# Optimization experiments

Measured on AMD Instinct MI355X. Metric: run time of the kernel, lower is better.

## Reference

```python
import jax, jax.numpy as jnp
import numpy as np

N = 10000
IN_DIM = 1024
HID = 128
LAT = 64
E = 320000


def setup_inputs() -> dict:
    key = jax.random.key(0)
    ks = jax.random.split(key, 12)
    def glorot(k, shape):
        lim = float(np.sqrt(6.0 / (shape[0] + shape[1])))
        return jax.random.uniform(k, shape, jnp.float32, -lim, lim)
    x = jax.random.normal(ks[0], (N, IN_DIM), jnp.float32)
    edge_index = jax.random.randint(ks[1], (2, E), 0, N, jnp.int64)
    return {
        "x": x,
        "edge_index": edge_index,
        "W_enc1": glorot(ks[2], (IN_DIM, HID)), "b_enc1": jnp.zeros((HID,), jnp.float32),
        "W_enc2": glorot(ks[3], (HID, LAT)),   "b_enc2": jnp.zeros((LAT,), jnp.float32),
        "W_att1": glorot(ks[4], (LAT, HID)),   "b_att1": jnp.zeros((HID,), jnp.float32),
        "W_att2": glorot(ks[5], (HID, IN_DIM)),"b_att2": jnp.zeros((IN_DIM,), jnp.float32),
        "W_str":  glorot(ks[6], (LAT, LAT)),   "b_str":  jnp.zeros((LAT,), jnp.float32),
    }


def _gcn_norm(edge_index, n):
    # PyG GCNConv default: add self-loops, symmetric normalization
    loop = jnp.arange(n, dtype=edge_index.dtype)
    send = jnp.concatenate([edge_index[0], loop])
    recv = jnp.concatenate([edge_index[1], loop])
    deg = jax.ops.segment_sum(jnp.ones_like(recv, dtype=jnp.float32), recv, num_segments=n)
    dis = jnp.where(deg > 0, jax.lax.rsqrt(deg), 0.0)
    norm = dis[send] * dis[recv]  # [E+N]
    return send, recv, norm


def _gcn(x, W, b, send, recv, norm, n):
    h = x @ W                                  # [N, out]
    msg = h[send] * norm[:, None]              # gather + scale
    agg = jax.ops.segment_sum(msg, recv, num_segments=n)  # scatter-add
    return agg + b


def reference(x, edge_index, W_enc1, b_enc1, W_enc2, b_enc2,
              W_att1, b_att1, W_att2, b_att2, W_str, b_str):
    n = x.shape[0]
    send, recv, norm = _gcn_norm(edge_index, n)
    # encoder
    h = jax.nn.relu(_gcn(x, W_enc1, b_enc1, send, recv, norm, n))
    z = jax.nn.relu(_gcn(h, W_enc2, b_enc2, send, recv, norm, n))
    # attribute decoder
    a = jax.nn.relu(_gcn(z, W_att1, b_att1, send, recv, norm, n))
    attr_recon = jax.nn.relu(_gcn(a, W_att2, b_att2, send, recv, norm, n))
    # structure decoder
    s = jax.nn.relu(_gcn(z, W_str, b_str, send, recv, norm, n))
    struct_recon = s @ s.T  # [N, N]
    return (attr_recon, struct_recon, z)
```

## Files before the change

### kernel.cpp

```cpp
#include <hip/hip_runtime.h>
#include <hip/hip_bf16.h>

#define IN_DIM 1024
#define HID 128
#define LAT 64
#define DEGPAD 128

typedef __attribute__((ext_vector_type(8))) short bf16x8;
typedef __attribute__((ext_vector_type(4))) short bf16x4;
typedef __attribute__((ext_vector_type(4))) float f32x4;

#define W1T_OFF 0
#define W2T_OFF 131072
#define Wa1T_OFF 139264
#define Wa2T_OFF 147456
#define WsT_OFF 278528
#define WT_TOTAL 282624

__device__ __forceinline__ void splitf(float v, __hip_bfloat16& h, __hip_bfloat16& l) {
    h = __float2bfloat16(v);
    l = __float2bfloat16(v - __bfloat162float(h));
}


template<int AMODE, bool BIAS, bool RELU, bool DIS, bool SPLITOUT, bool NT>
__device__ void dev_gemm(float* smem, int bx, int byy,
        const __hip_bfloat16* __restrict__ Ahi, const __hip_bfloat16* __restrict__ Alo,
        const float* __restrict__ Af,
        const __hip_bfloat16* __restrict__ Bthi, const __hip_bfloat16* __restrict__ Btlo,
        const float* __restrict__ bias, const int* __restrict__ cursor,
        float* __restrict__ Cf, __hip_bfloat16* __restrict__ Chi, __hip_bfloat16* __restrict__ Clo,
        int M, int K, int ldc) {
    int tid = threadIdx.x;
    int w = tid >> 6, lane = tid & 63;
    int wr = w >> 1, wc = w & 1;
    int m0 = byy * 128, n0 = bx * 64;
    int lrow = lane & 15, lk = (lane >> 4) * 8;

    int arow[4];
    size_t aoff[4];
#pragma unroll
    for (int mi = 0; mi < 4; ++mi) {
        arow[mi] = m0 + wr * 64 + mi * 16 + lrow;
        aoff[mi] = (size_t)arow[mi] * K + lk;
    }
    size_t boff[2];
#pragma unroll
    for (int nj = 0; nj < 2; ++nj)
        boff[nj] = (size_t)(n0 + wc * 32 + nj * 16 + lrow) * K + lk;

    f32x4 acc[4][2] = {};

    for (int k0 = 0; k0 < K; k0 += 32) {
        bf16x8 bh[2], bl[2], ah[4], al[4];
#pragma unroll
        for (int nj = 0; nj < 2; ++nj) {
            bh[nj] = *(const bf16x8*)(Bthi + boff[nj] + k0);
            bl[nj] = *(const bf16x8*)(Btlo + boff[nj] + k0);
        }
        if constexpr (AMODE == 0) {
#pragma unroll
            for (int mi = 0; mi < 4; ++mi) {
                ah[mi] = *(const bf16x8*)(Ahi + aoff[mi] + k0);
                al[mi] = *(const bf16x8*)(Alo + aoff[mi] + k0);
            }
        } else {
#pragma unroll
            for (int mi = 0; mi < 4; ++mi) {
                float4 f0 = make_float4(0.f, 0.f, 0.f, 0.f), f1 = f0;
                if (arow[mi] < M) {
                    f0 = *(const float4*)(Af + aoff[mi] + k0);
                    f1 = *(const float4*)(Af + aoff[mi] + k0 + 4);
                }
                float ff[8] = {f0.x, f0.y, f0.z, f0.w, f1.x, f1.y, f1.z, f1.w};
                __attribute__((aligned(16))) __hip_bfloat16 hb[8], lb[8];
#pragma unroll
                for (int t = 0; t < 8; ++t) splitf(ff[t], hb[t], lb[t]);
                ah[mi] = *(const bf16x8*)hb;
                al[mi] = *(const bf16x8*)lb;
            }
        }
#pragma unroll
        for (int mi = 0; mi < 4; ++mi)
#pragma unroll
            for (int nj = 0; nj < 2; ++nj) {
                acc[mi][nj] = __builtin_amdgcn_mfma_f32_16x16x32_bf16(ah[mi], bh[nj], acc[mi][nj], 0, 0, 0);
                acc[mi][nj] = __builtin_amdgcn_mfma_f32_16x16x32_bf16(ah[mi], bl[nj], acc[mi][nj], 0, 0, 0);
                acc[mi][nj] = __builtin_amdgcn_mfma_f32_16x16x32_bf16(al[mi], bh[nj], acc[mi][nj], 0, 0, 0);
            }
    }

    int r0 = (lane >> 4) * 4;
#pragma unroll
    for (int mi = 0; mi < 4; ++mi)
#pragma unroll
        for (int nj = 0; nj < 2; ++nj) {
            int cl = wc * 32 + nj * 16 + lrow;
#pragma unroll
            for (int r = 0; r < 4; ++r) {
                int rl = wr * 64 + mi * 16 + r0 + r;
                smem[rl * 68 + cl] = acc[mi][nj][r];
            }
        }
    __syncthreads();

#pragma unroll
    for (int it = 0; it < 8; ++it) {
        int rl = it * 16 + (tid >> 4);
        int c4 = tid & 15;
        int row = m0 + rl;
        if (row < M) {
            int col = n0 + c4 * 4;
            float4 v = *(const float4*)&smem[rl * 68 + c4 * 4];
            if (BIAS) {
                float4 b = *(const float4*)&bias[col];
                v.x += b.x; v.y += b.y; v.z += b.z; v.w += b.w;
            }
            if (RELU) {
                v.x = fmaxf(v.x, 0.f); v.y = fmaxf(v.y, 0.f);
                v.z = fmaxf(v.z, 0.f); v.w = fmaxf(v.w, 0.f);
            }
            if (DIS) {
                float di = rsqrtf((float)(cursor[row] + 1));
                v.x *= di; v.y *= di; v.z *= di; v.w *= di;
            }
            if constexpr (SPLITOUT) {
                float vv[4] = {v.x, v.y, v.z, v.w};
                __attribute__((aligned(8))) __hip_bfloat16 hs[4], ls[4];
#pragma unroll
                for (int k = 0; k < 4; ++k) splitf(vv[k], hs[k], ls[k]);
                *(bf16x4*)&Chi[(size_t)row * ldc + col] = *(bf16x4*)hs;
                *(bf16x4*)&Clo[(size_t)row * ldc + col] = *(bf16x4*)ls;
            } else if constexpr (NT) {
                __builtin_nontemporal_store(*(const f32x4*)&v, (f32x4*)&Cf[(size_t)row * ldc + col]);
            } else {
                *(float4*)&Cf[(size_t)row * ldc + col] = v;
            }
        }
    }
    __syncthreads();
}


__device__ void dev_sst(float* smem, int bi, int bj,
                        const __hip_bfloat16* __restrict__ Shi, const __hip_bfloat16* __restrict__ Slo,
                        float* __restrict__ C, int M) {
    int tid = threadIdx.x;
    int w = tid >> 6, lane = tid & 63;
    int wr = w >> 1, wc = w & 1;
    int i0 = bi * 128 + wr * 64;
    int j0 = bj * 128 + wc * 64;
    int lrow = lane & 15, lk = (lane >> 4) * 8;

    f32x4 acc[4][4] = {};
#pragma unroll
    for (int ks = 0; ks < 2; ++ks) {
        bf16x8 ah[4], al[4], bh[4], bl[4];
#pragma unroll
        for (int mi = 0; mi < 4; ++mi) {
            size_t off = (size_t)(i0 + mi * 16 + lrow) * 64 + ks * 32 + lk;
            ah[mi] = *(const bf16x8*)(Shi + off);
            al[mi] = *(const bf16x8*)(Slo + off);
        }
#pragma unroll
        for (int nj = 0; nj < 4; ++nj) {
            size_t off = (size_t)(j0 + nj * 16 + lrow) * 64 + ks * 32 + lk;
            bh[nj] = *(const bf16x8*)(Shi + off);
            bl[nj] = *(const bf16x8*)(Slo + off);
        }
#pragma unroll
        for (int mi = 0; mi < 4; ++mi)
#pragma unroll
            for (int nj = 0; nj < 4; ++nj) {
                acc[mi][nj] = __builtin_amdgcn_mfma_f32_16x16x32_bf16(ah[mi], bh[nj], acc[mi][nj], 0, 0, 0);
                acc[mi][nj] = __builtin_amdgcn_mfma_f32_16x16x32_bf16(ah[mi], bl[nj], acc[mi][nj], 0, 0, 0);
                acc[mi][nj] = __builtin_amdgcn_mfma_f32_16x16x32_bf16(al[mi], bh[nj], acc[mi][nj], 0, 0, 0);
            }
    }

    int r0 = (lane >> 4) * 4;

    if (bi != bj) {
#pragma unroll
        for (int mi = 0; mi < 4; ++mi)
#pragma unroll
            for (int nj = 0; nj < 4; ++nj) {
                int orow = j0 + nj * 16 + lrow;
                int ocol = i0 + mi * 16 + r0;
                if (orow < M && ocol < M) {
                    f32x4 v = acc[mi][nj];
                    __builtin_nontemporal_store(v, (f32x4*)&C[(size_t)orow * M + ocol]);
                }
            }
    }

#pragma unroll
    for (int p = 0; p < 2; ++p) {
        if (wc == p) {
#pragma unroll
            for (int mi = 0; mi < 4; ++mi)
#pragma unroll
                for (int nj = 0; nj < 4; ++nj) {
                    int cl = nj * 16 + lrow;
#pragma unroll
                    for (int r = 0; r < 4; ++r) {
                        int rl = wr * 64 + mi * 16 + r0 + r;
                        smem[rl * 68 + cl] = acc[mi][nj][r];
                    }
                }
        }
        __syncthreads();
#pragma unroll
        for (int it = 0; it < 8; ++it) {
            int rl = it * 16 + (tid >> 4);
            int c4 = tid & 15;
            int row = bi * 128 + rl;
            int col = bj * 128 + p * 64 + c4 * 4;
            if (row < M && col < M) {
                float4 v = *(const float4*)&smem[rl * 68 + c4 * 4];
                __builtin_nontemporal_store(*(const f32x4*)&v, (f32x4*)&C[(size_t)row * M + col]);
            }
        }
        __syncthreads();
    }
}


__global__ __launch_bounds__(256) void k_prep(const float* __restrict__ W1, const float* __restrict__ W2,
                                              const float* __restrict__ Wa1, const float* __restrict__ Wa2,
                                              const float* __restrict__ Ws,
                                              __hip_bfloat16* __restrict__ hi, __hip_bfloat16* __restrict__ lo,
                                              int* cursor, int N) {
    int gtid = blockIdx.x * 256 + threadIdx.x;
    int gsz = gridDim.x * 256;
    for (int i = gtid; i < N; i += gsz) cursor[i] = 0;
    for (int idx = gtid; idx < WT_TOTAL; idx += gsz) {
        const float* src; int base, shK, Nc;
        if (idx < W2T_OFF)       { src = W1;  base = W1T_OFF;  shK = 10; Nc = 128; }
        else if (idx < Wa1T_OFF) { src = W2;  base = W2T_OFF;  shK = 7;  Nc = 64; }
        else if (idx < Wa2T_OFF) { src = Wa1; base = Wa1T_OFF; shK = 6;  Nc = 128; }
        else if (idx < WsT_OFF)  { src = Wa2; base = Wa2T_OFF; shK = 7;  Nc = 1024; }
        else                     { src = Ws;  base = WsT_OFF;  shK = 6;  Nc = 64; }
        int local = idx - base;
        int nn = local >> shK;
        int k = local & ((1 << shK) - 1);
        splitf(src[(size_t)k * Nc + nn], hi[idx], lo[idx]);
    }
}

__global__ __launch_bounds__(256) void k_build(const int* __restrict__ ei, int* cursor,
                                               int* __restrict__ colPad, int E,
                                               const float* __restrict__ x,
                                               const __hip_bfloat16* __restrict__ Whi,
                                               const __hip_bfloat16* __restrict__ Wlo,
                                               float* __restrict__ t128, int M, int Mpad) {
    __shared__ float smem[128 * 68];
    int gtid = blockIdx.x * 256 + threadIdx.x;
    int gsz = gridDim.x * 256;
    for (int e = gtid; e < E; e += gsz) {
        int s = ei[e], r = ei[E + e];
        int slot = atomicAdd(&cursor[r], 1);
        if (slot < DEGPAD) colPad[(size_t)r * DEGPAD + slot] = s;
    }
    int nt2 = (Mpad / 128) * 2;
    for (int t = blockIdx.x; t < nt2; t += gridDim.x)
        dev_gemm<1, false, false, false, false, false>(smem, t & 1, t >> 1,
            nullptr, nullptr, x, Whi + W1T_OFF, Wlo + W1T_OFF, nullptr, nullptr,
            t128, nullptr, nullptr, M, 1024, 128);
}

template<int F, bool BIAS, bool RELU, int OMODE, bool GD>
__global__ __launch_bounds__(256) void k_spmm(const float* __restrict__ Hin,
                                              const int* __restrict__ colPad,
                                              const int* __restrict__ cursor,
                                              const float* __restrict__ bias,
                                              float* __restrict__ out, float* __restrict__ out2,
                                              __hip_bfloat16* __restrict__ ohi,
                                              __hip_bfloat16* __restrict__ olo, int n) {
    constexpr int JW = F / 64;
    int i = (blockIdx.x * 256 + threadIdx.x) >> 6;
    int lane = threadIdx.x & 63;
    if (i >= n) return;
    int d = cursor[i];
    float di = rsqrtf((float)(d + 1));
    if (d > DEGPAD) d = DEGPAD;
    const int* cp = colPad + (size_t)i * DEGPAD;
    float acc[JW];
    const float* self = Hin + (size_t)i * F;
#pragma unroll
    for (int j = 0; j < JW; ++j) acc[j] = (GD ? di : 1.f) * self[lane + 64 * j];

    int p = 0;
    for (; p + 4 <= d; p += 4) {
        int4 cidx = *(const int4*)(cp + p);
        int cc[4] = {cidx.x, cidx.y, cidx.z, cidx.w};
        float dc[4];
        if constexpr (GD) {
#pragma unroll
            for (int q = 0; q < 4; ++q) dc[q] = rsqrtf((float)(cursor[cc[q]] + 1));
        }
        float vals[4][JW];
#pragma unroll
        for (int q = 0; q < 4; ++q) {
            const float* row = Hin + (size_t)cc[q] * F;
#pragma unroll
            for (int j = 0; j < JW; ++j) vals[q][j] = row[lane + 64 * j];
        }
#pragma unroll
        for (int q = 0; q < 4; ++q)
#pragma unroll
            for (int j = 0; j < JW; ++j)
                acc[j] = GD ? fmaf(dc[q], vals[q][j], acc[j]) : (acc[j] + vals[q][j]);
    }
    for (; p < d; ++p) {
        int c = cp[p];
        const float* row = Hin + (size_t)c * F;
        if constexpr (GD) {
            float dc = rsqrtf((float)(cursor[c] + 1));
#pragma unroll
            for (int j = 0; j < JW; ++j) acc[j] = fmaf(dc, row[lane + 64 * j], acc[j]);
        } else {
#pragma unroll
            for (int j = 0; j < JW; ++j) acc[j] += row[lane + 64 * j];
        }
    }

#pragma unroll
    for (int j = 0; j < JW; ++j) {
        float r = acc[j] * di;
        if (BIAS) r += bias[lane + 64 * j];
        if (RELU) r = fmaxf(r, 0.f);
        size_t idx = (size_t)i * F + lane + 64 * j;
        if constexpr (OMODE == 1) {
            __hip_bfloat16 h, l;
            splitf(r, h, l);
            ohi[idx] = h; olo[idx] = l;
        } else {
            out[idx] = r;
            if constexpr (OMODE == 2) out2[idx] = r * di;
        }
    }
}

__global__ __launch_bounds__(256) void k_g2(const __hip_bfloat16* __restrict__ Hhi,
                                            const __hip_bfloat16* __restrict__ Hlo,
                                            const __hip_bfloat16* __restrict__ Whi,
                                            const __hip_bfloat16* __restrict__ Wlo,
                                            const int* __restrict__ cursor,
                                            float* __restrict__ t64, int M) {
    __shared__ float smem[128 * 68];
    dev_gemm<0, false, false, true, false, false>(smem, 0, blockIdx.x,
        Hhi, Hlo, nullptr, Whi + W2T_OFF, Wlo + W2T_OFF, nullptr, cursor,
        t64, nullptr, nullptr, M, 128, 64);
}

__global__ __launch_bounds__(256) void k_g34(const __hip_bfloat16* __restrict__ AZhi,
                                             const __hip_bfloat16* __restrict__ AZlo,
                                             const __hip_bfloat16* __restrict__ Whi,
                                             const __hip_bfloat16* __restrict__ Wlo,
                                             const float* __restrict__ ba1, const float* __restrict__ bs,
                                             const int* __restrict__ cursor,
                                             float* __restrict__ t128,
                                             __hip_bfloat16* __restrict__ Shi, __hip_bfloat16* __restrict__ Slo,
                                             int M, int Mpad) {
    __shared__ float smem[128 * 68];
    int nt2 = (Mpad / 128) * 2;
    int t = blockIdx.x;
    if (t < nt2)
        dev_gemm<0, true, true, true, false, false>(smem, t & 1, t >> 1,
            AZhi, AZlo, nullptr, Whi + Wa1T_OFF, Wlo + Wa1T_OFF, ba1, cursor,
            t128, nullptr, nullptr, M, 64, 128);
    else
        dev_gemm<0, true, true, false, true, false>(smem, 0, t - nt2,
            AZhi, AZlo, nullptr, Whi + WsT_OFF, Wlo + WsT_OFF, bs, nullptr,
            nullptr, Shi, Slo, M, 64, 64);
}

__global__ __launch_bounds__(256) void k_tail(const __hip_bfloat16* __restrict__ AAhi,
                                              const __hip_bfloat16* __restrict__ AAlo,
                                              const __hip_bfloat16* __restrict__ Whi,
                                              const __hip_bfloat16* __restrict__ Wlo,
                                              const float* __restrict__ ba2,
                                              const __hip_bfloat16* __restrict__ Shi,
                                              const __hip_bfloat16* __restrict__ Slo,
                                              float* __restrict__ attr, float* __restrict__ st,
                                              int M, int Mpad) {
    __shared__ float smem[128 * 68];
    int nt = Mpad / 128;
    int nG5 = 16 * nt;
    int t = blockIdx.x;
    if (t < nG5) {
        dev_gemm<0, true, true, false, false, true>(smem, t & 15, t >> 4,
            AAhi, AAlo, nullptr, Whi + Wa2T_OFF, Wlo + Wa2T_OFF, ba2, nullptr,
            attr, nullptr, nullptr, M, 128, 1024);
    } else {
        int tt = t - nG5;
        int bi = 0;
        while (tt >= nt - bi) { tt -= nt - bi; bi++; }
        dev_sst(smem, bi, bi + tt, Shi, Slo, st, M);
    }
}


extern "C" void kernel_launch(void* const* d_in, const int* in_sizes, int n_in,
                              void* d_out, int out_size, void* d_ws, size_t ws_size,
                              hipStream_t stream) {
    const float* x   = (const float*)d_in[0];
    const int*   ei  = (const int*)d_in[1];
    const float* W1  = (const float*)d_in[2];
    const float* b1  = (const float*)d_in[3];
    const float* W2  = (const float*)d_in[4];
    const float* b2  = (const float*)d_in[5];
    const float* Wa1 = (const float*)d_in[6];
    const float* ba1 = (const float*)d_in[7];
    const float* Wa2 = (const float*)d_in[8];
    const float* ba2 = (const float*)d_in[9];
    const float* Ws  = (const float*)d_in[10];
    const float* bs  = (const float*)d_in[11];

    int N = in_sizes[0] / IN_DIM;
    int E = in_sizes[1] / 2;
    int Mpad = ((N + 127) / 128) * 128;
    int nt = Mpad / 128;

    float* out  = (float*)d_out;
    float* attr = out;
    float* st   = out + (size_t)N * IN_DIM;
    float* zout = st + (size_t)N * N;

    char* basep = (char*)d_ws;
    size_t off = 0;
    auto alloc = [&](size_t bytes) -> void* {
        void* p = basep + off;
        off = (off + bytes + 255) & ~(size_t)255;
        return p;
    };
    int*   colPad = (int*)alloc((size_t)N * DEGPAD * 4);
    int*   cursor = (int*)alloc((size_t)N * 4);
    __hip_bfloat16* Whi = (__hip_bfloat16*)alloc((size_t)WT_TOTAL * 2);
    __hip_bfloat16* Wlo = (__hip_bfloat16*)alloc((size_t)WT_TOTAL * 2);
    float* t128 = (float*)alloc((size_t)N * 128 * 4);
    float* t64  = (float*)alloc((size_t)N * 64 * 4);
    float* zp   = (float*)alloc((size_t)N * 64 * 4);
    __hip_bfloat16* Hhi  = (__hip_bfloat16*)alloc((size_t)Mpad * 128 * 2);
    __hip_bfloat16* Hlo  = (__hip_bfloat16*)alloc((size_t)Mpad * 128 * 2);
    __hip_bfloat16* AZhi = (__hip_bfloat16*)alloc((size_t)Mpad * 64 * 2);
    __hip_bfloat16* AZlo = (__hip_bfloat16*)alloc((size_t)Mpad * 64 * 2);
    __hip_bfloat16* AAhi = (__hip_bfloat16*)alloc((size_t)Mpad * 128 * 2);
    __hip_bfloat16* AAlo = (__hip_bfloat16*)alloc((size_t)Mpad * 128 * 2);
    __hip_bfloat16* Shi  = (__hip_bfloat16*)alloc((size_t)Mpad * 64 * 2);
    __hip_bfloat16* Slo  = (__hip_bfloat16*)alloc((size_t)Mpad * 64 * 2);

    dim3 b256(256);
    int spmm_grid = (N * 64 + 255) / 256;

    k_prep<<<dim3(1104), b256, 0, stream>>>(W1, W2, Wa1, Wa2, Ws, Whi, Wlo, cursor, N);
    k_build<<<dim3(1280), b256, 0, stream>>>(ei, cursor, colPad, E, x, Whi, Wlo, t128, N, Mpad);
    k_spmm<128, true, true, 1, true><<<dim3(spmm_grid), b256, 0, stream>>>(
        t128, colPad, cursor, b1, nullptr, nullptr, Hhi, Hlo, N);
    k_g2<<<dim3(nt), b256, 0, stream>>>(Hhi, Hlo, Whi, Wlo, cursor, t64, N);
    k_spmm<64, true, true, 2, false><<<dim3(spmm_grid), b256, 0, stream>>>(
        t64, colPad, cursor, b2, zout, zp, nullptr, nullptr, N);
    k_spmm<64, false, false, 1, false><<<dim3(spmm_grid), b256, 0, stream>>>(
        zp, colPad, cursor, nullptr, nullptr, nullptr, AZhi, AZlo, N);
    k_g34<<<dim3(3 * nt), b256, 0, stream>>>(AZhi, AZlo, Whi, Wlo, ba1, bs, cursor, t128, Shi, Slo, N, Mpad);
    k_spmm<128, false, false, 1, false><<<dim3(spmm_grid), b256, 0, stream>>>(
        t128, colPad, cursor, nullptr, nullptr, nullptr, AAhi, AAlo, N);
    k_tail<<<dim3(16 * nt + nt * (nt + 1) / 2), b256, 0, stream>>>(
        AAhi, AAlo, Whi, Wlo, ba2, Shi, Slo, attr, st, N, Mpad);
}
```

Before: 300.0 us.

## Move edge CSR build into prep and fold degree scaling into first GEMM epilogue

The edge bucketing with atomics moves from the build kernel into the weight-prep kernel, and the cursor zeroing becomes a memset. The first layer's GEMM becomes its own kernel that applies the source-degree scale through its epilogue (the flag that takes cursor). This removes the per-neighbour rsqrt and cursor gather from the first SpMM. The SpMM also gets an 8-wide unrolled gather loop for more memory-level parallelism. It costs an extra launch and a stricter ordering between the CSR build and the GEMM.

Result: no change. 299.7 us (median of 2 runs) (-0.1%).

```diff
diff --git a/kernel.cpp b/kernel.cpp
--- a/kernel.cpp
+++ b/kernel.cpp
@@ -230,10 +230,15 @@
                                               const float* __restrict__ Wa1, const float* __restrict__ Wa2,
                                               const float* __restrict__ Ws,
                                               __hip_bfloat16* __restrict__ hi, __hip_bfloat16* __restrict__ lo,
-                                              int* cursor, int N) {
+                                              const int* __restrict__ ei, int* cursor,
+                                              int* __restrict__ colPad, int E) {
     int gtid = blockIdx.x * 256 + threadIdx.x;
     int gsz = gridDim.x * 256;
-    for (int i = gtid; i < N; i += gsz) cursor[i] = 0;
+    for (int e = gtid; e < E; e += gsz) {
+        int s = ei[e], r = ei[E + e];
+        int slot = atomicAdd(&cursor[r], 1);
+        if (slot < DEGPAD) colPad[(size_t)r * DEGPAD + slot] = s;
+    }
     for (int idx = gtid; idx < WT_TOTAL; idx += gsz) {
         const float* src; int base, shK, Nc;
         if (idx < W2T_OFF)       { src = W1;  base = W1T_OFF;  shK = 10; Nc = 128; }
@@ -248,28 +253,19 @@
     }
 }
 
-__global__ __launch_bounds__(256) void k_build(const int* __restrict__ ei, int* cursor,
-                                               int* __restrict__ colPad, int E,
-                                               const float* __restrict__ x,
-                                               const __hip_bfloat16* __restrict__ Whi,
-                                               const __hip_bfloat16* __restrict__ Wlo,
-                                               float* __restrict__ t128, int M, int Mpad) {
+__global__ __launch_bounds__(256) void k_g1(const float* __restrict__ x,
+                                            const __hip_bfloat16* __restrict__ Whi,
+                                            const __hip_bfloat16* __restrict__ Wlo,
+                                            const int* __restrict__ cursor,
+                                            float* __restrict__ t128, int M) {
     __shared__ float smem[128 * 68];
-    int gtid = blockIdx.x * 256 + threadIdx.x;
-    int gsz = gridDim.x * 256;
-    for (int e = gtid; e < E; e += gsz) {
-        int s = ei[e], r = ei[E + e];
-        int slot = atomicAdd(&cursor[r], 1);
-        if (slot < DEGPAD) colPad[(size_t)r * DEGPAD + slot] = s;
-    }
-    int nt2 = (Mpad / 128) * 2;
-    for (int t = blockIdx.x; t < nt2; t += gridDim.x)
-        dev_gemm<1, false, false, false, false, false>(smem, t & 1, t >> 1,
-            nullptr, nullptr, x, Whi + W1T_OFF, Wlo + W1T_OFF, nullptr, nullptr,
-            t128, nullptr, nullptr, M, 1024, 128);
-}
-
-template<int F, bool BIAS, bool RELU, int OMODE, bool GD>
+    int t = blockIdx.x;
+    dev_gemm<1, false, false, true, false, false>(smem, t & 1, t >> 1,
+        nullptr, nullptr, x, Whi + W1T_OFF, Wlo + W1T_OFF, nullptr, cursor,
+        t128, nullptr, nullptr, M, 1024, 128);
+}
+
+template<int F, bool BIAS, bool RELU, int OMODE>
 __global__ __launch_bounds__(256) void k_spmm(const float* __restrict__ Hin,
                                               const int* __restrict__ colPad,
                                               const int* __restrict__ cursor,
@@ -288,17 +284,28 @@
     float acc[JW];
     const float* self = Hin + (size_t)i * F;
 #pragma unroll
-    for (int j = 0; j < JW; ++j) acc[j] = (GD ? di : 1.f) * self[lane + 64 * j];
+    for (int j = 0; j < JW; ++j) acc[j] = self[lane + 64 * j];
 
     int p = 0;
+    for (; p + 8 <= d; p += 8) {
+        int4 ca = *(const int4*)(cp + p);
+        int4 cb = *(const int4*)(cp + p + 4);
+        int cc[8] = {ca.x, ca.y, ca.z, ca.w, cb.x, cb.y, cb.z, cb.w};
+        float vals[8][JW];
+#pragma unroll
+        for (int q = 0; q < 8; ++q) {
+            const float* row = Hin + (size_t)cc[q] * F;
+#pragma unroll
+            for (int j = 0; j < JW; ++j) vals[q][j] = row[lane + 64 * j];
+        }
+#pragma unroll
+        for (int q = 0; q < 8; ++q)
+#pragma unroll
+            for (int j = 0; j < JW; ++j) acc[j] += vals[q][j];
+    }
     for (; p + 4 <= d; p += 4) {
-        int4 cidx = *(const int4*)(cp + p);
-        int cc[4] = {cidx.x, cidx.y, cidx.z, cidx.w};
-        float dc[4];
-        if constexpr (GD) {
-#pragma unroll
-            for (int q = 0; q < 4; ++q) dc[q] = rsqrtf((float)(cursor[cc[q]] + 1));
-        }
+        int4 ca = *(const int4*)(cp + p);
+        int cc[4] = {ca.x, ca.y, ca.z, ca.w};
         float vals[4][JW];
 #pragma unroll
         for (int q = 0; q < 4; ++q) {
@@ -309,20 +316,12 @@
 #pragma unroll
         for (int q = 0; q < 4; ++q)
 #pragma unroll
-            for (int j = 0; j < JW; ++j)
-                acc[j] = GD ? fmaf(dc[q], vals[q][j], acc[j]) : (acc[j] + vals[q][j]);
+            for (int j = 0; j < JW; ++j) acc[j] += vals[q][j];
     }
     for (; p < d; ++p) {
-        int c = cp[p];
-        const float* row = Hin + (size_t)c * F;
-        if constexpr (GD) {
-            float dc = rsqrtf((float)(cursor[c] + 1));
-#pragma unroll
-            for (int j = 0; j < JW; ++j) acc[j] = fmaf(dc, row[lane + 64 * j], acc[j]);
-        } else {
-#pragma unroll
-            for (int j = 0; j < JW; ++j) acc[j] += row[lane + 64 * j];
-        }
+        const float* row = Hin + (size_t)cp[p] * F;
+#pragma unroll
+        for (int j = 0; j < JW; ++j) acc[j] += row[lane + 64 * j];
     }
 
 #pragma unroll
@@ -454,17 +453,18 @@
     dim3 b256(256);
     int spmm_grid = (N * 64 + 255) / 256;
 
-    k_prep<<<dim3(1104), b256, 0, stream>>>(W1, W2, Wa1, Wa2, Ws, Whi, Wlo, cursor, N);
-    k_build<<<dim3(1280), b256, 0, stream>>>(ei, cursor, colPad, E, x, Whi, Wlo, t128, N, Mpad);
-    k_spmm<128, true, true, 1, true><<<dim3(spmm_grid), b256, 0, stream>>>(
+    hipMemsetAsync(cursor, 0, (size_t)N * 4, stream);
+    k_prep<<<dim3(1280), b256, 0, stream>>>(W1, W2, Wa1, Wa2, Ws, Whi, Wlo, ei, cursor, colPad, E);
+    k_g1<<<dim3(2 * nt), b256, 0, stream>>>(x, Whi, Wlo, cursor, t128, N);
+    k_spmm<128, true, true, 1><<<dim3(spmm_grid), b256, 0, stream>>>(
         t128, colPad, cursor, b1, nullptr, nullptr, Hhi, Hlo, N);
     k_g2<<<dim3(nt), b256, 0, stream>>>(Hhi, Hlo, Whi, Wlo, cursor, t64, N);
-    k_spmm<64, true, true, 2, false><<<dim3(spmm_grid), b256, 0, stream>>>(
+    k_spmm<64, true, true, 2><<<dim3(spmm_grid), b256, 0, stream>>>(
         t64, colPad, cursor, b2, zout, zp, nullptr, nullptr, N);
-    k_spmm<64, false, false, 1, false><<<dim3(spmm_grid), b256, 0, stream>>>(
+    k_spmm<64, false, false, 1><<<dim3(spmm_grid), b256, 0, stream>>>(
         zp, colPad, cursor, nullptr, nullptr, nullptr, AZhi, AZlo, N);
     k_g34<<<dim3(3 * nt), b256, 0, stream>>>(AZhi, AZlo, Whi, Wlo, ba1, bs, cursor, t128, Shi, Slo, N, Mpad);
-    k_spmm<128, false, false, 1, false><<<dim3(spmm_grid), b256, 0, stream>>>(
+    k_spmm<128, false, false, 1><<<dim3(spmm_grid), b256, 0, stream>>>(
         t128, colPad, cursor, nullptr, nullptr, nullptr, AAhi, AAlo, N);
     k_tail<<<dim3(16 * nt + nt * (nt + 1) / 2), b256, 0, stream>>>(
         AAhi, AAlo, Whi, Wlo, ba2, Shi, Slo, attr, st, N, Mpad);
```
